# Optimization experiments

Hardware: AMD Instinct MI355X
Metric: run time of the kernel (lower is better)

Reference implementation:

```python
import jax, jax.numpy as jnp
import numpy as np

B, S, D, H, DH, L, MLP, VOCAB = 1, 2048, 512, 8, 64, 6, 2048, 256
BLOCK, C = 128, 32
EPS = 1e-6
NEG = -1e9


def layer_norm(x, scale, bias):
    mu = jnp.mean(x, axis=-1, keepdims=True)
    var = jnp.mean(jnp.square(x - mu), axis=-1, keepdims=True)
    return (x - mu) * jax.lax.rsqrt(var + EPS) * scale + bias


def sparse_pattern_mask(seq_len):
    # Union of Fixed1 (same causal block) and Fixed2 (last c columns of each
    # block), both intersected with the causal mask. Shape [S, S] bool.
    i = jnp.arange(seq_len)[:, None]
    j = jnp.arange(seq_len)[None, :]
    causal = j <= i
    fixed1 = (i // BLOCK) == (j // BLOCK)
    fixed2 = (j % BLOCK) >= (BLOCK - C)
    return causal & (fixed1 | fixed2)


def setup_inputs() -> dict:
    key = jax.random.key(0)
    ks = jax.random.split(key, 12)
    s = 0.02
    inp = {
        'tokens': jax.random.randint(ks[0], (B, S), 0, VOCAB, dtype=jnp.int32),
        'embed': jax.random.normal(ks[1], (VOCAB, D), jnp.float32) * s,
        'pos_emb': jax.random.normal(ks[2], (1, S, D), jnp.float32) * s,
        'ln1_scale': jnp.ones((L, D), jnp.float32),
        'ln1_bias': jnp.zeros((L, D), jnp.float32),
        'wq': jax.random.normal(ks[3], (L, D, H, DH), jnp.float32) * s,
        'wk': jax.random.normal(ks[4], (L, D, H, DH), jnp.float32) * s,
        'wv': jax.random.normal(ks[5], (L, D, H, DH), jnp.float32) * s,
        'wo': jax.random.normal(ks[6], (L, H, DH, D), jnp.float32) * s,
        'ln2_scale': jnp.ones((L, D), jnp.float32),
        'ln2_bias': jnp.zeros((L, D), jnp.float32),
        'w1': jax.random.normal(ks[7], (L, D, MLP), jnp.float32) * s,
        'b1': jnp.zeros((L, MLP), jnp.float32),
        'w2': jax.random.normal(ks[8], (L, MLP, D), jnp.float32) * s,
        'b2': jnp.zeros((L, D), jnp.float32),
        'lnf_scale': jnp.ones((D,), jnp.float32),
        'lnf_bias': jnp.zeros((D,), jnp.float32),
        'wout': jax.random.normal(ks[9], (D, VOCAB), jnp.float32) * s,
        'bout': jnp.zeros((VOCAB,), jnp.float32),
    }
    return inp


def _forward(tokens, embed, pos_emb, ln1_scale, ln1_bias, wq, wk, wv, wo,
             ln2_scale, ln2_bias, w1, b1, w2, b2, lnf_scale, lnf_bias,
             wout, bout):
    # padding mask computed on unshifted inputs (keys with token==0 are masked)
    key_pad = tokens > 0                               # [B, S]
    # shift right (decoder teacher forcing)
    shifted = jnp.pad(tokens, ((0, 0), (1, 0)))[:, :-1]
    x = embed[shifted] + pos_emb                       # [B, S, D]

    pattern = sparse_pattern_mask(S)                   # [S, S]
    mask = pattern[None, None] & key_pad[:, None, None, :]  # [B,1,S,S]

    for l in range(L):
        h = layer_norm(x, ln1_scale[l], ln1_bias[l])
        q = jnp.einsum('bsd,dhk->bshk', h, wq[l]) / jnp.sqrt(
            jnp.asarray(DH, x.dtype))
        k = jnp.einsum('bsd,dhk->bshk', h, wk[l])
        v = jnp.einsum('bsd,dhk->bshk', h, wv[l])
        scores = jnp.einsum('bqhk,bshk->bhqs', q, k)   # [B,H,S,S]
        scores = jnp.where(mask, scores, NEG)
        probs = jax.nn.softmax(scores, axis=-1)
        o = jnp.einsum('bhqs,bshk->bqhk', probs, v)
        x = x + jnp.einsum('bqhk,hkd->bqd', o, wo[l])

        y = layer_norm(x, ln2_scale[l], ln2_bias[l])
        y = jax.nn.gelu(y @ w1[l] + b1[l])
        x = x + (y @ w2[l] + b2[l])

    x = layer_norm(x, lnf_scale, lnf_bias)
    return x @ wout + bout                             # [B, S, VOCAB]


def reference(tokens, embed, pos_emb, ln1_scale, ln1_bias, wq, wk, wv, wo,
              ln2_scale, ln2_bias, w1, b1, w2, b2, lnf_scale, lnf_bias,
              wout, bout):
    return _forward(tokens, embed, pos_emb, ln1_scale, ln1_bias, wq, wk, wv,
                    wo, ln2_scale, ln2_bias, w1, b1, w2, b2, lnf_scale,
                    lnf_bias, wout, bout)
```

## Files before the change

### kernel.cpp

```cpp
#include <hip/hip_runtime.h>
#include <hip/hip_bf16.h>
#include <cstdint>
#include <cstddef>

#define DEV __device__ __forceinline__

namespace {

constexpr int S    = 2048;
constexpr int D    = 512;
constexpr int H    = 8;
constexpr int DH   = 64;
constexpr int NL   = 6;
constexpr int MLPD = 2048;
constexpr int VOC  = 256;
constexpr int QS   = 1536;
constexpr float EPSF = 1e-6f;

typedef unsigned short u16;
typedef __attribute__((ext_vector_type(8))) short s8v;
typedef __attribute__((ext_vector_type(4))) float f4v;

DEV float u2f(u16 u){
  union { unsigned int i; float f; } t; t.i = ((unsigned int)u) << 16; return t.f;
}
DEV short bfr(float f){
  __hip_bfloat16 h = __float2bfloat16(f);
  short s; __builtin_memcpy(&s, &h, 2); return s;
}
DEV float gelu_fast(float x){
  float z = 0.7978845608028654f * (x + 0.044715f * x * x * x);
  return x / (1.f + __expf(-2.f * z));
}
DEV void gll16(const u16* gp, u16* lp){
  __builtin_amdgcn_global_load_lds(
      (const __attribute__((address_space(1))) unsigned int*)gp,
      (__attribute__((address_space(3))) unsigned int*)lp, 16, 0, 0);
}

__global__ void k_embed(const int* __restrict__ tokens, const float* __restrict__ emb,
                        const float* __restrict__ pos, float* __restrict__ x){
  int s = blockIdx.x;
  int tok = (s == 0) ? 0 : tokens[s - 1];
  if (tok < 0) tok = 0; if (tok >= VOC) tok = VOC - 1;
  const float* er = emb + (size_t)tok * D;
  const float* pr = pos + (size_t)s * D;
  float* xr = x + (size_t)s * D;
  for (int d = threadIdx.x; d < D; d += blockDim.x)
    xr[d] = er[d] + pr[d];
}

template<int HASP>
__global__ __launch_bounds__(256)
void k_lnr(const float* __restrict__ P0, const float* __restrict__ P1,
           const float* __restrict__ bias, float* __restrict__ x,
           const float* __restrict__ sc, const float* __restrict__ bi,
           u16* __restrict__ out)
{
  int s = blockIdx.x * 4 + (threadIdx.x >> 6), t = threadIdx.x & 63;
  size_t base = (size_t)s * D;
  float v[8]; float sum = 0.f, sq = 0.f;
  #pragma unroll
  for (int e = 0; e < 8; ++e){
    int d = t + 64 * e;
    size_t idx = base + d;
    float xv = x[idx];
    if (HASP){
      float bv = bias ? bias[d] : 0.f;
      xv += P0[idx] + P1[idx] + bv;
      x[idx] = xv;
    }
    v[e] = xv; sum += xv; sq += xv * xv;
  }
  #pragma unroll
  for (int off = 32; off >= 1; off >>= 1){
    sum += __shfl_down(sum, off, 64);
    sq  += __shfl_down(sq,  off, 64);
  }
  sum = __shfl(sum, 0, 64); sq = __shfl(sq, 0, 64);
  float mu  = sum * (1.f / (float)D);
  float var = sq * (1.f / (float)D) - mu * mu;
  float r = rsqrtf(var + EPSF);
  u16* orow = out + base;
  #pragma unroll
  for (int e = 0; e < 8; ++e){
    int d = t + 64 * e;
    orow[d] = (u16)bfr((v[e] - mu) * r * sc[d] + bi[d]);
  }
}

__global__ __launch_bounds__(256)
void k_wt(const float* __restrict__ src, u16* __restrict__ dst, int R, int C,
          size_t sStr, size_t dStr){
  src += (size_t)blockIdx.z * sStr;
  dst += (size_t)blockIdx.z * dStr;
  __shared__ float tb[32][33];
  int c0 = blockIdx.x * 32, r0 = blockIdx.y * 32;
  int tc = threadIdx.x & 31, tr8 = threadIdx.x >> 5;
  #pragma unroll
  for (int rr = 0; rr < 32; rr += 8)
    tb[rr + tr8][tc] = src[(size_t)(r0 + rr + tr8) * C + c0 + tc];
  __syncthreads();
  #pragma unroll
  for (int rr = 0; rr < 32; rr += 8)
    dst[(size_t)(c0 + rr + tr8) * R + r0 + tc] = (u16)bfr(tb[tc][rr + tr8]);
}

__global__ __launch_bounds__(256)
void k_wt4(const float* __restrict__ wq, const float* __restrict__ wk,
           const float* __restrict__ wv, const float* __restrict__ wo,
           u16* __restrict__ wqkvT, u16* __restrict__ woT)
{
  const size_t L512 = (size_t)512 * 512;
  int fam = blockIdx.z / 6, l = blockIdx.z % 6;
  const float* src;
  u16* dst;
  if (fam == 0){ src = wq + (size_t)l * L512; dst = wqkvT + (size_t)l * QS * 512; }
  else if (fam == 1){ src = wk + (size_t)l * L512; dst = wqkvT + (size_t)l * QS * 512 + 512 * 512; }
  else if (fam == 2){ src = wv + (size_t)l * L512; dst = wqkvT + (size_t)l * QS * 512 + 1024 * 512; }
  else { src = wo + (size_t)l * L512; dst = woT + (size_t)l * L512; }
  __shared__ float tb[32][33];
  int c0 = blockIdx.x * 32, r0 = blockIdx.y * 32;
  int tc = threadIdx.x & 31, tr8 = threadIdx.x >> 5;
  #pragma unroll
  for (int rr = 0; rr < 32; rr += 8)
    tb[rr + tr8][tc] = src[(size_t)(r0 + rr + tr8) * 512 + c0 + tc];
  __syncthreads();
  #pragma unroll
  for (int rr = 0; rr < 32; rr += 8)
    dst[(size_t)(c0 + rr + tr8) * 512 + r0 + tc] = (u16)bfr(tb[tc][rr + tr8]);
}

template<int FM, int FN, int MODE>
__global__ __launch_bounds__(64)
void k_gd(const u16* __restrict__ A, const u16* __restrict__ Bt,
          const float* __restrict__ bias, float* __restrict__ Cf,
          u16* __restrict__ Cb, int N, int K, float alpha)
{
  const int nx = gridDim.x;
  const int nwg = nx * gridDim.y;
  int wg = blockIdx.y * nx + blockIdx.x;
  wg = (wg & 7) * (nwg >> 3) + (wg >> 3);
  const int m0 = (wg / nx) * (FM * 16), n0 = (wg % nx) * (FN * 16);
  const int lane = threadIdx.x, lr = lane & 15, lg = lane >> 4;
  const u16* ap = A  + (size_t)(m0 + lr) * K + lg * 8;
  const u16* bp = Bt + (size_t)(n0 + lr) * K + lg * 8;
  f4v acc[FM][FN] = {};
  #pragma unroll 4
  for (int k0 = 0; k0 < K; k0 += 32){
    s8v af[FM], bf[FN];
    #pragma unroll
    for (int fi = 0; fi < FM; ++fi)
      af[fi] = *reinterpret_cast<const s8v*>(ap + (size_t)fi * 16 * K + k0);
    #pragma unroll
    for (int fj = 0; fj < FN; ++fj)
      bf[fj] = *reinterpret_cast<const s8v*>(bp + (size_t)fj * 16 * K + k0);
    #pragma unroll
    for (int fi = 0; fi < FM; ++fi)
      #pragma unroll
      for (int fj = 0; fj < FN; ++fj)
        acc[fi][fj] = __builtin_amdgcn_mfma_f32_16x16x32_bf16(af[fi], bf[fj], acc[fi][fj], 0, 0, 0);
  }
  #pragma unroll
  for (int fi = 0; fi < FM; ++fi)
    #pragma unroll
    for (int fj = 0; fj < FN; ++fj)
      #pragma unroll
      for (int r = 0; r < 4; ++r){
        int row = m0 + fi * 16 + lg * 4 + r;
        int col = n0 + fj * 16 + lr;
        size_t idx = (size_t)row * N + col;
        float v = acc[fi][fj][r];
        if (MODE == 1)      Cb[idx] = (u16)bfr(gelu_fast(v + bias[col]));
        else if (MODE == 2) Cf[idx] += v + (bias ? bias[col] : 0.f);
        else if (MODE == 3) Cf[idx] = v + bias[col];
        else {
          float al = (col < 512) ? alpha : 1.f;
          Cb[idx] = (u16)bfr(v * al);
        }
      }
}

template<int MODE>
__global__ __launch_bounds__(256)
void k_gs(const u16* __restrict__ A, const u16* __restrict__ Bt,
          const float* __restrict__ bias, u16* __restrict__ Cb,
          int N, int K)
{
  __shared__ __align__(16) u16 As[128 * 32];
  __shared__ __align__(16) u16 Bs[64 * 32];
  const int nx = gridDim.x;
  const int nwg = nx * gridDim.y;
  int wg = blockIdx.y * nx + blockIdx.x;
  wg = (wg & 7) * (nwg >> 3) + (wg >> 3);
  const int m0 = (wg / nx) * 128, n0 = (wg % nx) * 64;
  const int w = threadIdx.x >> 6, lane = threadIdx.x & 63;
  const int lr = lane & 15, lg = lane >> 4;
  const int wr = w >> 1, wc = w & 1;
  const int srow = lane >> 2, scd = lane & 3;
  const int swA0 = ((srow) ^ (srow >> 2)) & 3;
  f4v acc[4][2] = {};
  for (int k0 = 0; k0 < K; k0 += 32){
    __syncthreads();
    #pragma unroll
    for (int j = w; j < 8; j += 4){
      int row = j * 16 + srow;
      int g = scd ^ swA0;
      gll16(A + (size_t)(m0 + row) * K + k0 + g * 8, As + j * 512);
    }
    {
      int row = w * 16 + srow;
      int g = scd ^ swA0;
      gll16(Bt + (size_t)(n0 + row) * K + k0 + g * 8, Bs + w * 512);
    }
    asm volatile("s_waitcnt vmcnt(0)" ::: "memory");
    __syncthreads();
    s8v af[4], bf[2];
    #pragma unroll
    for (int fi = 0; fi < 4; ++fi){
      int row = wr * 64 + fi * 16 + lr;
      int slot = lg ^ ((row ^ (row >> 2)) & 3);
      af[fi] = *reinterpret_cast<const s8v*>(As + row * 32 + slot * 8);
    }
    #pragma unroll
    for (int fj = 0; fj < 2; ++fj){
      int row = wc * 32 + fj * 16 + lr;
      int slot = lg ^ ((row ^ (row >> 2)) & 3);
      bf[fj] = *reinterpret_cast<const s8v*>(Bs + row * 32 + slot * 8);
    }
    #pragma unroll
    for (int fi = 0; fi < 4; ++fi)
      #pragma unroll
      for (int fj = 0; fj < 2; ++fj)
        acc[fi][fj] = __builtin_amdgcn_mfma_f32_16x16x32_bf16(af[fi], bf[fj], acc[fi][fj], 0, 0, 0);
  }
  #pragma unroll
  for (int fi = 0; fi < 4; ++fi)
    #pragma unroll
    for (int fj = 0; fj < 2; ++fj)
      #pragma unroll
      for (int r = 0; r < 4; ++r){
        int row = m0 + wr * 64 + fi * 16 + lg * 4 + r;
        int col = n0 + wc * 32 + fj * 16 + lr;
        float v = acc[fi][fj][r];
        if (MODE == 1) Cb[(size_t)row * N + col] = (u16)bfr(gelu_fast(v + bias[col]));
      }
}

__global__ __launch_bounds__(256)
void k_gsq(const u16* __restrict__ A, const u16* __restrict__ Bt,
           u16* __restrict__ vt, u16* __restrict__ Cb, float alpha)
{
  constexpr int K = 512, N = QS;
  __shared__ __align__(16) u16 As[128 * 32];
  __shared__ __align__(16) u16 Bs[64 * 32];
  const int nx = gridDim.x;
  const int nwg = nx * gridDim.y;
  int wg = blockIdx.y * nx + blockIdx.x;
  wg = (wg & 7) * (nwg >> 3) + (wg >> 3);
  const int m0 = (wg / nx) * 128, n0 = (wg % nx) * 64;
  const int w = threadIdx.x >> 6, lane = threadIdx.x & 63;
  const int lr = lane & 15, lg = lane >> 4;
  const int wr = w >> 1, wc = w & 1;
  const int srow = lane >> 2, scd = lane & 3;
  const int swA0 = ((srow) ^ (srow >> 2)) & 3;
  f4v acc[4][2] = {};
  for (int k0 = 0; k0 < K; k0 += 32){
    __syncthreads();
    #pragma unroll
    for (int j = w; j < 8; j += 4){
      int row = j * 16 + srow;
      int g = scd ^ swA0;
      gll16(A + (size_t)(m0 + row) * K + k0 + g * 8, As + j * 512);
    }
    {
      int row = w * 16 + srow;
      int g = scd ^ swA0;
      gll16(Bt + (size_t)(n0 + row) * K + k0 + g * 8, Bs + w * 512);
    }
    asm volatile("s_waitcnt vmcnt(0)" ::: "memory");
    __syncthreads();
    s8v af[4], bf[2];
    #pragma unroll
    for (int fi = 0; fi < 4; ++fi){
      int row = wr * 64 + fi * 16 + lr;
      int slot = lg ^ ((row ^ (row >> 2)) & 3);
      af[fi] = *reinterpret_cast<const s8v*>(As + row * 32 + slot * 8);
    }
    #pragma unroll
    for (int fj = 0; fj < 2; ++fj){
      int row = wc * 32 + fj * 16 + lr;
      int slot = lg ^ ((row ^ (row >> 2)) & 3);
      bf[fj] = *reinterpret_cast<const s8v*>(Bs + row * 32 + slot * 8);
    }
    #pragma unroll
    for (int fi = 0; fi < 4; ++fi)
      #pragma unroll
      for (int fj = 0; fj < 2; ++fj)
        acc[fi][fj] = __builtin_amdgcn_mfma_f32_16x16x32_bf16(af[fi], bf[fj], acc[fi][fj], 0, 0, 0);
  }
  #pragma unroll
  for (int fi = 0; fi < 4; ++fi)
    #pragma unroll
    for (int fj = 0; fj < 2; ++fj)
      #pragma unroll
      for (int r = 0; r < 4; ++r){
        int row = m0 + wr * 64 + fi * 16 + lg * 4 + r;
        int col = n0 + wc * 32 + fj * 16 + lr;
        float v = acc[fi][fj][r];
        if (col < 512){
          Cb[(size_t)row * N + col] = (u16)bfr(v * alpha);
        } else if (col < 1024){
          Cb[(size_t)row * N + col] = (u16)bfr(v);
        } else {
          vt[(size_t)(col - 1024) * S + row] = (u16)bfr(v);
        }
      }
}

template<int FM, int FN>
__global__ __launch_bounds__(64)
void k_gds(const u16* __restrict__ A, const u16* __restrict__ Bt,
           float* __restrict__ P, int N, int K, int KC)
{
  const int nx = gridDim.x;
  const int nwg = nx * gridDim.y;
  const int M = gridDim.y * (FM * 16);
  int wg = blockIdx.y * nx + blockIdx.x;
  wg = (wg & 7) * (nwg >> 3) + (wg >> 3);
  const int m0 = (wg / nx) * (FM * 16), n0 = (wg % nx) * (FN * 16);
  const int z = blockIdx.z;
  const int lane = threadIdx.x, lr = lane & 15, lg = lane >> 4;
  const u16* ap = A  + (size_t)(m0 + lr) * K + z * KC + lg * 8;
  const u16* bp = Bt + (size_t)(n0 + lr) * K + z * KC + lg * 8;
  P += (size_t)z * M * N;
  f4v acc[FM][FN] = {};
  #pragma unroll 4
  for (int k0 = 0; k0 < KC; k0 += 32){
    s8v af[FM], bf[FN];
    #pragma unroll
    for (int fi = 0; fi < FM; ++fi)
      af[fi] = *reinterpret_cast<const s8v*>(ap + (size_t)fi * 16 * K + k0);
    #pragma unroll
    for (int fj = 0; fj < FN; ++fj)
      bf[fj] = *reinterpret_cast<const s8v*>(bp + (size_t)fj * 16 * K + k0);
    #pragma unroll
    for (int fi = 0; fi < FM; ++fi)
      #pragma unroll
      for (int fj = 0; fj < FN; ++fj)
        acc[fi][fj] = __builtin_amdgcn_mfma_f32_16x16x32_bf16(af[fi], bf[fj], acc[fi][fj], 0, 0, 0);
  }
  #pragma unroll
  for (int fi = 0; fi < FM; ++fi)
    #pragma unroll
    for (int fj = 0; fj < FN; ++fj)
      #pragma unroll
      for (int r = 0; r < 4; ++r){
        int row = m0 + fi * 16 + lg * 4 + r;
        int col = n0 + fj * 16 + lr;
        P[(size_t)row * N + col] = acc[fi][fj][r];
      }
}

__global__ __launch_bounds__(64)
void k_mattn(const u16* __restrict__ qp_, const u16* __restrict__ kp_,
             const u16* __restrict__ vt, const int* __restrict__ tokens,
             u16* __restrict__ ob)
{
  const int q0 = (gridDim.x - 1 - blockIdx.x) * 16;
  const int h  = blockIdx.y;
  const int B  = q0 >> 7;
  const int lane = threadIdx.x, lr = lane & 15, lg = lane >> 4;

  __shared__ __align__(16) u16 Ps[16][40];

  const u16* qrow = qp_ + (size_t)(q0 + lr) * QS + h * DH;
  s8v qf0 = *reinterpret_cast<const s8v*>(qrow + lg * 8);
  s8v qf1 = *reinterpret_cast<const s8v*>(qrow + 32 + lg * 8);

  f4v o0 = {}, o1 = {}, o2 = {}, o3 = {};
  float m[4] = {-1e30f, -1e30f, -1e30f, -1e30f};
  float l[4] = {0.f, 0.f, 0.f, 0.f};

  const int ntiles = B + ((q0 & 127) >> 5) + 1;

  for (int tt = 0; tt < ntiles; ++tt){
    int kbase; bool causal;
    if (tt < B){ kbase = tt * 128 + 96; causal = false; }
    else       { kbase = B * 128 + (tt - B) * 32; causal = (kbase + 31 > q0); }

    f4v s0 = {}, s1 = {};
    const u16* k0p = kp_ + (size_t)(kbase + lr) * QS + h * DH;
    const u16* k1p = kp_ + (size_t)(kbase + 16 + lr) * QS + h * DH;
    s8v kf;
    kf = *reinterpret_cast<const s8v*>(k0p + lg * 8);
    s0 = __builtin_amdgcn_mfma_f32_16x16x32_bf16(qf0, kf, s0, 0, 0, 0);
    kf = *reinterpret_cast<const s8v*>(k0p + 32 + lg * 8);
    s0 = __builtin_amdgcn_mfma_f32_16x16x32_bf16(qf1, kf, s0, 0, 0, 0);
    kf = *reinterpret_cast<const s8v*>(k1p + lg * 8);
    s1 = __builtin_amdgcn_mfma_f32_16x16x32_bf16(qf0, kf, s1, 0, 0, 0);
    kf = *reinterpret_cast<const s8v*>(k1p + 32 + lg * 8);
    s1 = __builtin_amdgcn_mfma_f32_16x16x32_bf16(qf1, kf, s1, 0, 0, 0);

    const int tok0 = tokens[kbase + lr] > 0;
    const int tok1 = tokens[kbase + 16 + lr] > 0;
    #pragma unroll
    for (int r = 0; r < 4; ++r){
      int qg = q0 + 4 * lg + r;
      float a0 = (tok0 && (!causal || kbase + lr <= qg))      ? s0[r] : -1e30f;
      float a1 = (tok1 && (!causal || kbase + 16 + lr <= qg)) ? s1[r] : -1e30f;
      float tm = fmaxf(a0, a1);
      tm = fmaxf(tm, __shfl_xor(tm, 1, 64));
      tm = fmaxf(tm, __shfl_xor(tm, 2, 64));
      tm = fmaxf(tm, __shfl_xor(tm, 4, 64));
      tm = fmaxf(tm, __shfl_xor(tm, 8, 64));
      float mn = fmaxf(m[r], tm);
      bool dead = (mn <= -1e29f);
      float sc = dead ? 1.f : __expf(m[r] - mn);
      float p0 = dead ? 0.f : __expf(a0 - mn);
      float p1 = dead ? 0.f : __expf(a1 - mn);
      l[r] = l[r] * sc + p0 + p1;
      m[r] = mn;
      o0[r] *= sc; o1[r] *= sc; o2[r] *= sc; o3[r] *= sc;
      Ps[4 * lg + r][lr]      = (u16)bfr(p0);
      Ps[4 * lg + r][16 + lr] = (u16)bfr(p1);
    }

    asm volatile("s_waitcnt lgkmcnt(0)" ::: "memory");
    __builtin_amdgcn_sched_barrier(0);
    s8v pf  = *reinterpret_cast<const s8v*>(&Ps[lr][lg * 8]);
    const u16* vtb = vt + (size_t)(h * DH + lr) * S + kbase + lg * 8;
    s8v vf0 = *reinterpret_cast<const s8v*>(vtb);
    s8v vf1 = *reinterpret_cast<const s8v*>(vtb + (size_t)16 * S);
    s8v vf2 = *reinterpret_cast<const s8v*>(vtb + (size_t)32 * S);
    s8v vf3 = *reinterpret_cast<const s8v*>(vtb + (size_t)48 * S);
    o0 = __builtin_amdgcn_mfma_f32_16x16x32_bf16(pf, vf0, o0, 0, 0, 0);
    o1 = __builtin_amdgcn_mfma_f32_16x16x32_bf16(pf, vf1, o1, 0, 0, 0);
    o2 = __builtin_amdgcn_mfma_f32_16x16x32_bf16(pf, vf2, o2, 0, 0, 0);
    o3 = __builtin_amdgcn_mfma_f32_16x16x32_bf16(pf, vf3, o3, 0, 0, 0);
  }

  #pragma unroll
  for (int r = 0; r < 4; ++r){
    float lt = l[r];
    lt += __shfl_xor(lt, 1, 64);
    lt += __shfl_xor(lt, 2, 64);
    lt += __shfl_xor(lt, 4, 64);
    lt += __shfl_xor(lt, 8, 64);
    int qg = q0 + 4 * lg + r;
    u16* orow = ob + (size_t)qg * D + h * DH;
    if (lt <= 0.f){
      #pragma unroll
      for (int c4 = 0; c4 < 4; ++c4){
        const u16* vr = vt + (size_t)(h * DH + c4 * 16 + lr) * S;
        float s = 0.f;
        for (int j = 0; j < S; ++j) s += u2f(vr[j]);
        orow[c4 * 16 + lr] = (u16)bfr(s * (1.f / (float)S));
      }
    } else {
      float inv = 1.f / lt;
      orow[lr]      = (u16)bfr(o0[r] * inv);
      orow[16 + lr] = (u16)bfr(o1[r] * inv);
      orow[32 + lr] = (u16)bfr(o2[r] * inv);
      orow[48 + lr] = (u16)bfr(o3[r] * inv);
    }
  }
}

}

extern "C" void kernel_launch(void* const* d_in, const int* in_sizes, int n_in,
                              void* d_out, int out_size, void* d_ws, size_t ws_size,
                              hipStream_t stream)
{
  (void)n_in; (void)out_size; (void)ws_size;

  int I_tok=0, I_emb=1, I_pos=2, I_l1s=3, I_l1b=4, I_wq=5, I_wk=6, I_wv=7,
      I_wo=8, I_l2s=9, I_l2b=10, I_w1=11, I_b1=12, I_w2=13, I_b2=14,
      I_lfs=15, I_lfb=16, I_wout=17, I_bout=18;
  if (in_sizes[0] != S){
    I_b1=0;  I_b2=1;  I_bout=2; I_emb=3;  I_l1b=4; I_l1s=5;  I_l2b=6;
    I_l2s=7; I_lfb=8; I_lfs=9;  I_pos=10; I_tok=11; I_w1=12; I_w2=13;
    I_wk=14; I_wo=15; I_wout=16; I_wq=17; I_wv=18;
  }

  const int*   tokens = (const int*)d_in[I_tok];
  const float* emb  = (const float*)d_in[I_emb];
  const float* pos  = (const float*)d_in[I_pos];
  const float* ln1s = (const float*)d_in[I_l1s];
  const float* ln1b = (const float*)d_in[I_l1b];
  const float* wq   = (const float*)d_in[I_wq];
  const float* wk   = (const float*)d_in[I_wk];
  const float* wv   = (const float*)d_in[I_wv];
  const float* wo   = (const float*)d_in[I_wo];
  const float* ln2s = (const float*)d_in[I_l2s];
  const float* ln2b = (const float*)d_in[I_l2b];
  const float* w1   = (const float*)d_in[I_w1];
  const float* b1   = (const float*)d_in[I_b1];
  const float* w2   = (const float*)d_in[I_w2];
  const float* b2   = (const float*)d_in[I_b2];
  const float* lnfs = (const float*)d_in[I_lfs];
  const float* lnfb = (const float*)d_in[I_lfb];
  const float* wout = (const float*)d_in[I_wout];
  const float* bout = (const float*)d_in[I_bout];
  float* outp = (float*)d_out;

  char* ws = (char*)d_ws;
  float* x    = (float*)(ws);
  u16*  hb    = (u16*)(ws + ((size_t)4  << 20));
  u16*  qkvb  = (u16*)(ws + ((size_t)6  << 20));
  u16*  ob    = (u16*)(ws + ((size_t)12 << 20));
  u16*  gb    = (u16*)(ws + ((size_t)14 << 20));
  u16*  vtb   = (u16*)(ws + ((size_t)14 << 20));
  float* pWO  = (float*)(ws + ((size_t)14 << 20));
  float* pW2  = (float*)(ws + ((size_t)6  << 20));
  u16*  wqkvT = (u16*)(ws + ((size_t)23 << 20));
  u16*  w1T   = (u16*)(ws + ((size_t)32 << 20));
  u16*  w2T   = (u16*)(ws + ((size_t)44 << 20));
  u16*  woT   = (u16*)(ws + ((size_t)56 << 20));
  u16*  woutT = (u16*)(ws + ((size_t)59 << 20));

  const size_t L512 = (size_t)512 * 512;
  const size_t LMLP = (size_t)512 * 2048;
  const size_t SM   = (size_t)S * 512;

  k_wt4<<<dim3(16, 16, 24), dim3(256), 0, stream>>>(wq, wk, wv, wo, wqkvT, woT);
  k_wt<<<dim3(64, 16, 6), dim3(256), 0, stream>>>(w1, w1T, 512, 2048, LMLP, LMLP);
  k_wt<<<dim3(16, 64, 6), dim3(256), 0, stream>>>(w2, w2T, 2048, 512, LMLP, LMLP);
  k_wt<<<dim3(8,  16, 1), dim3(256), 0, stream>>>(wout, woutT, 512, 256, 0, 0);

  k_embed<<<dim3(S), dim3(128), 0, stream>>>(tokens, emb, pos, x);

  for (int l = 0; l < NL; ++l){
    if (l == 0){
      k_lnr<0><<<dim3(S/4), dim3(256), 0, stream>>>(
          nullptr, nullptr, nullptr, x, ln1s, ln1b, hb);
    }
    k_gsq<<<dim3(24, 16), dim3(256), 0, stream>>>(
        hb, wqkvT + (size_t)l * QS * 512, vtb, qkvb, 0.125f);
    k_mattn<<<dim3(S/16, H), dim3(64), 0, stream>>>(
        qkvb, qkvb + 512, vtb, tokens, ob);
    k_gds<2,4><<<dim3(8, 64, 2), dim3(64), 0, stream>>>(
        ob, woT + (size_t)l * L512, pWO, 512, 512, 256);
    k_lnr<1><<<dim3(S/4), dim3(256), 0, stream>>>(
        pWO, pWO + SM, nullptr, x, ln2s + (size_t)l*D, ln2b + (size_t)l*D, hb);
    k_gs<1><<<dim3(32, 16), dim3(256), 0, stream>>>(
        hb, w1T + (size_t)l * LMLP, b1 + (size_t)l*MLPD, gb, MLPD, 512);
    k_gds<2,4><<<dim3(8, 64, 2), dim3(64), 0, stream>>>(
        gb, w2T + (size_t)l * LMLP, pW2, 512, 2048, 1024);
    if (l < NL - 1){
      k_lnr<1><<<dim3(S/4), dim3(256), 0, stream>>>(
          pW2, pW2 + SM, b2 + (size_t)l*D, x,
          ln1s + (size_t)(l+1)*D, ln1b + (size_t)(l+1)*D, hb);
    } else {
      k_lnr<1><<<dim3(S/4), dim3(256), 0, stream>>>(
          pW2, pW2 + SM, b2 + (size_t)l*D, x, lnfs, lnfb, hb);
    }
  }

  k_gd<2,4,3><<<dim3(4, 64), dim3(64), 0, stream>>>(
      hb, woutT, bout, outp, nullptr, VOC, 512, 1.f);
}
```

Baseline: 689.6 us.

## Split attention key tiles across two wavefronts and merge softmax states

```diff
diff --git a/kernel.cpp b/kernel.cpp
--- a/kernel.cpp
+++ b/kernel.cpp
@@ -362,7 +362,7 @@
       }
 }
 
-__global__ __launch_bounds__(64)
+__global__ __launch_bounds__(128)
 void k_mattn(const u16* __restrict__ qp_, const u16* __restrict__ kp_,
              const u16* __restrict__ vt, const int* __restrict__ tokens,
              u16* __restrict__ ob)
@@ -370,9 +370,11 @@
   const int q0 = (gridDim.x - 1 - blockIdx.x) * 16;
   const int h  = blockIdx.y;
   const int B  = q0 >> 7;
-  const int lane = threadIdx.x, lr = lane & 15, lg = lane >> 4;
-
-  __shared__ __align__(16) u16 Ps[16][40];
+  const int w  = threadIdx.x >> 6;
+  const int lane = threadIdx.x & 63, lr = lane & 15, lg = lane >> 4;
+
+  __shared__ __align__(16) u16 Ps[2][16][40];
+  __shared__ float Msh[64][4], Lsh[64][4], Osh[4][64][4];
 
   const u16* qrow = qp_ + (size_t)(q0 + lr) * QS + h * DH;
   s8v qf0 = *reinterpret_cast<const s8v*>(qrow + lg * 8);
@@ -384,7 +386,7 @@
 
   const int ntiles = B + ((q0 & 127) >> 5) + 1;
 
-  for (int tt = 0; tt < ntiles; ++tt){
+  for (int tt = w; tt < ntiles; tt += 2){
     int kbase; bool causal;
     if (tt < B){ kbase = tt * 128 + 96; causal = false; }
     else       { kbase = B * 128 + (tt - B) * 32; causal = (kbase + 31 > q0); }
@@ -422,13 +424,13 @@
       l[r] = l[r] * sc + p0 + p1;
       m[r] = mn;
       o0[r] *= sc; o1[r] *= sc; o2[r] *= sc; o3[r] *= sc;
-      Ps[4 * lg + r][lr]      = (u16)bfr(p0);
-      Ps[4 * lg + r][16 + lr] = (u16)bfr(p1);
+      Ps[w][4 * lg + r][lr]      = (u16)bfr(p0);
+      Ps[w][4 * lg + r][16 + lr] = (u16)bfr(p1);
     }
 
     asm volatile("s_waitcnt lgkmcnt(0)" ::: "memory");
     __builtin_amdgcn_sched_barrier(0);
-    s8v pf  = *reinterpret_cast<const s8v*>(&Ps[lr][lg * 8]);
+    s8v pf  = *reinterpret_cast<const s8v*>(&Ps[w][lr][lg * 8]);
     const u16* vtb = vt + (size_t)(h * DH + lr) * S + kbase + lg * 8;
     s8v vf0 = *reinterpret_cast<const s8v*>(vtb);
     s8v vf1 = *reinterpret_cast<const s8v*>(vtb + (size_t)16 * S);
@@ -438,6 +440,35 @@
     o1 = __builtin_amdgcn_mfma_f32_16x16x32_bf16(pf, vf1, o1, 0, 0, 0);
     o2 = __builtin_amdgcn_mfma_f32_16x16x32_bf16(pf, vf2, o2, 0, 0, 0);
     o3 = __builtin_amdgcn_mfma_f32_16x16x32_bf16(pf, vf3, o3, 0, 0, 0);
+  }
+
+  if (w == 1){
+    #pragma unroll
+    for (int r = 0; r < 4; ++r){
+      Msh[lane][r] = m[r];
+      Lsh[lane][r] = l[r];
+      Osh[0][lane][r] = o0[r];
+      Osh[1][lane][r] = o1[r];
+      Osh[2][lane][r] = o2[r];
+      Osh[3][lane][r] = o3[r];
+    }
+  }
+  __syncthreads();
+  if (w == 1) return;
+
+  #pragma unroll
+  for (int r = 0; r < 4; ++r){
+    float m1 = Msh[lane][r];
+    float M  = fmaxf(m[r], m1);
+    bool dead = (M <= -1e29f);
+    float f0 = dead ? 1.f : __expf(m[r] - M);
+    float f1 = dead ? 0.f : __expf(m1 - M);
+    l[r]  = l[r]  * f0 + Lsh[lane][r]    * f1;
+    o0[r] = o0[r] * f0 + Osh[0][lane][r] * f1;
+    o1[r] = o1[r] * f0 + Osh[1][lane][r] * f1;
+    o2[r] = o2[r] * f0 + Osh[2][lane][r] * f1;
+    o3[r] = o3[r] * f0 + Osh[3][lane][r] * f1;
+    m[r] = M;
   }
 
   #pragma unroll
@@ -538,7 +569,7 @@
     }
     k_gsq<<<dim3(24, 16), dim3(256), 0, stream>>>(
         hb, wqkvT + (size_t)l * QS * 512, vtb, qkvb, 0.125f);
-    k_mattn<<<dim3(S/16, H), dim3(64), 0, stream>>>(
+    k_mattn<<<dim3(S/16, H), dim3(128), 0, stream>>>(
         qkvb, qkvb + 512, vtb, tokens, ob);
     k_gds<2,4><<<dim3(8, 64, 2), dim3(64), 0, stream>>>(
         ob, woT + (size_t)l * L512, pWO, 512, 512, 256);
```

Result: faster. 634.1 us, median of 2 (-8.1%).
